# Kernel optimization log

Hardware: AMD Instinct MI355X
Metric: run time of the kernel (lower is better)

The kernel has to match this reference:

```python
import math
import jax, jax.numpy as jnp
import numpy as np

N_KV = 8
GROUP = 4
HEAD_DIM = 128
BATCH = 512
CACHE = 2048
CONTEXT = 4096
NEG_INF = -10000.0


def setup_inputs() -> dict:
    key = jax.random.key(0)
    k = jax.random.split(key, 6)
    queries = jax.random.normal(k[0], (N_KV * GROUP, BATCH, HEAD_DIM), jnp.float32)
    keys = jax.random.normal(k[1], (N_KV, BATCH, HEAD_DIM), jnp.float32)
    key_t_caches = jax.random.normal(k[2], (N_KV, HEAD_DIM, CACHE), jnp.float32)
    values = jax.random.normal(k[3], (N_KV, BATCH, HEAD_DIM), jnp.float32)
    value_caches = jax.random.normal(k[4], (N_KV, CACHE, HEAD_DIM), jnp.float32)
    # causal bias: token b (global position CACHE+b) may attend to positions <= CACHE+b;
    # padded tail [CACHE+BATCH, CONTEXT) is always masked with NEG_INF
    pos = jnp.arange(CONTEXT)[None, :]                       # [1, CONTEXT]
    limit = (CACHE + jnp.arange(BATCH))[:, None]             # [BATCH, 1]
    attn_bias = jnp.where(pos <= limit, 0.0, NEG_INF).astype(jnp.float32)
    kq_scale = jnp.asarray([1.0 / math.sqrt(HEAD_DIM)], jnp.float32)
    return {
        "queries": queries,
        "keys": keys,
        "key_t_caches": key_t_caches,
        "values": values,
        "value_caches": value_caches,
        "attn_bias": attn_bias,
        "kq_scale": kq_scale,
    }


def reference(queries, keys, key_t_caches, values, value_caches, attn_bias, kq_scale):
    n_kv, B, D = keys.shape
    n_heads = queries.shape[0]
    group = n_heads // n_kv
    cache = key_t_caches.shape[-1]
    context = attn_bias.shape[-1]
    pad = context - cache - B

    scaled_keys = keys * kq_scale                            # [kv, B, D]
    scaled_values = jnp.maximum(values, NEG_INF)             # [kv, B, D]

    # pad new keys/values to fill context, then prepend cache (matches torch pad+cat)
    padded_kt = jnp.pad(scaled_keys.transpose(0, 2, 1), ((0, 0), (0, 0), (0, pad)))
    all_keys_t = jnp.concatenate([key_t_caches, padded_kt], axis=-1)   # [kv, D, context]
    padded_v = jnp.pad(scaled_values, ((0, 0), (0, pad), (0, 0)))
    all_values = jnp.concatenate([value_caches, padded_v], axis=1)     # [kv, context, D]

    q = queries.reshape(n_kv, group, B, D)                   # group-major per kv head
    scores = jnp.einsum('kgbd,kdc->kgbc', q, all_keys_t) + attn_bias   # [kv, g, B, context]
    probs = jax.nn.softmax(scores, axis=-1)
    out = jnp.einsum('kgbc,kcd->kgbd', probs, all_values)    # [kv, g, B, D]
    head_outs = out.reshape(n_heads, B, D)
    return head_outs, scaled_keys, scaled_values
```

## Files before the change

### kernel.cpp

```cpp
#include <hip/hip_runtime.h>
#include <hip/hip_bf16.h>

#define NKV 8
#define NHEADS 32
#define HDIM 128
#define BATCH 512
#define CACHE 2048
#define CTX_TOT 2560
#define CT 64
#define SPLITS 6
#define KPITCH 128
#define VPITCH 64
#define PPITCH 72
#define NEG_BIG (-1e30f)

typedef __attribute__((ext_vector_type(8))) _Float16 half8;
typedef __attribute__((ext_vector_type(4))) float floatx4;

static __device__ __forceinline__ void dma16(const void* g, void* l) {
    __builtin_amdgcn_global_load_lds((const __attribute__((address_space(1))) void*)g,
                                     (__attribute__((address_space(3))) void*)l,
                                     16, 0, 0);
}

__global__ __launch_bounds__(256) void prep(const float* __restrict__ ktc,
                                            const float* __restrict__ vc,
                                            const float* __restrict__ keys,
                                            const float* __restrict__ values,
                                            const float* __restrict__ kq,
                                            float* __restrict__ outk,
                                            float* __restrict__ outv,
                                            _Float16* __restrict__ Kh,
                                            _Float16* __restrict__ Vth) {
    __shared__ float tile[128 * 33];
    const int bid = blockIdx.x;
    const int t = threadIdx.x;

    if (bid < 512) {
        int c0 = (bid & 63) * 32, kv = bid >> 6;
        const float* src = ktc + (size_t)kv * HDIM * CACHE + c0;
#pragma unroll
        for (int i = 0; i < 4; i++) {
            int idx = t + 256 * i;
            int d = idx >> 3, cc = idx & 7;
            float4 v = *(const float4*)(src + (size_t)d * CACHE + cc * 4);
            *(float4*)(&tile[d * 33 + cc * 4]) = v;
        }
        __syncthreads();
        _Float16* dst = Kh + ((size_t)kv * CTX_TOT + c0) * HDIM;
#pragma unroll
        for (int i = 0; i < 2; i++) {
            int c = (t >> 4) + 16 * i, dg = t & 15;
            half8 o;
#pragma unroll
            for (int k = 0; k < 8; k++) o[k] = (_Float16)tile[(dg * 8 + k) * 33 + c];
            *(half8*)(dst + (size_t)c * HDIM + dg * 8) = o;
        }
    } else if (bid < 1024) {
        int l = bid - 512;
        int c1 = (l & 15) * 128, d0 = ((l >> 4) & 3) * 32, kv = l >> 6;
        const float* src = vc + ((size_t)kv * CACHE + c1) * HDIM + d0;
#pragma unroll
        for (int i = 0; i < 4; i++) {
            int idx = t + 256 * i;
            int c = idx >> 3, dc = idx & 7;
            float4 v = *(const float4*)(src + (size_t)c * HDIM + dc * 4);
            *(float4*)(&tile[c * 33 + dc * 4]) = v;
        }
        __syncthreads();
        _Float16* dst = Vth + ((size_t)kv * HDIM + d0) * CTX_TOT + c1;
#pragma unroll
        for (int i = 0; i < 2; i++) {
            int d = (t >> 4) + 16 * i, cg = t & 15;
            half8 o;
#pragma unroll
            for (int k = 0; k < 8; k++) o[k] = (_Float16)tile[(cg * 8 + k) * 33 + d];
            *(half8*)(dst + (size_t)d * CTX_TOT + cg * 8) = o;
        }
    } else if (bid < 1536) {
        int base = ((bid - 1024) * 256 + t) * 4;
        float s = kq[0];
        float4 v = *(const float4*)(keys + base);
        v.x *= s; v.y *= s; v.z *= s; v.w *= s;
        *(float4*)(outk + base) = v;
        int kv = base >> 16;
        int rem = base & 0xFFFF;
        _Float16* dst = Kh + ((size_t)kv * CTX_TOT + CACHE) * HDIM + rem;
        dst[0] = (_Float16)v.x; dst[1] = (_Float16)v.y;
        dst[2] = (_Float16)v.z; dst[3] = (_Float16)v.w;
    } else {
        int l = bid - 1536;
        int b1 = (l & 3) * 128, d0 = ((l >> 2) & 3) * 32, kv = l >> 4;
        const float* src = values + ((size_t)kv * BATCH + b1) * HDIM + d0;
        float* dst32 = outv + ((size_t)kv * BATCH + b1) * HDIM + d0;
#pragma unroll
        for (int i = 0; i < 4; i++) {
            int idx = t + 256 * i;
            int b = idx >> 3, dc = idx & 7;
            float4 v = *(const float4*)(src + (size_t)b * HDIM + dc * 4);
            v.x = fmaxf(v.x, -10000.0f); v.y = fmaxf(v.y, -10000.0f);
            v.z = fmaxf(v.z, -10000.0f); v.w = fmaxf(v.w, -10000.0f);
            *(float4*)(dst32 + (size_t)b * HDIM + dc * 4) = v;
            *(float4*)(&tile[b * 33 + dc * 4]) = v;
        }
        __syncthreads();
        _Float16* dst = Vth + ((size_t)kv * HDIM + d0) * CTX_TOT + CACHE + b1;
#pragma unroll
        for (int i = 0; i < 2; i++) {
            int d = (t >> 4) + 16 * i, bg = t & 15;
            half8 o;
#pragma unroll
            for (int k = 0; k < 8; k++) o[k] = (_Float16)tile[(bg * 8 + k) * 33 + d];
            *(half8*)(dst + (size_t)d * CTX_TOT + bg * 8) = o;
        }
    }
}

__global__ __launch_bounds__(256, 3) void attn_split(const float* __restrict__ q_g,
                                                     const _Float16* __restrict__ Kh,
                                                     const _Float16* __restrict__ Vth,
                                                     _Float16* __restrict__ Opart,
                                                     float* __restrict__ MLpart) {
    __shared__ _Float16 Klds[CT * KPITCH];
    __shared__ _Float16 Vlds[HDIM * VPITCH];
    __shared__ _Float16 Plds[4][32 * PPITCH];

    const int h = blockIdx.x & 31;
    const int qb2 = blockIdx.x >> 5;
    const int s = blockIdx.y;
    const int kv = h >> 2;
    const int t = threadIdx.x;
    const int wave = t >> 6;
    const int lane = t & 63;
    const int l15 = lane & 15, quad = lane >> 4;

    const float LOG2E = 1.44269504088896340736f;
    const int qrow0 = qb2 * 128 + wave * 16;

    const _Float16* kg = Kh + (size_t)kv * CTX_TOT * HDIM;
    const _Float16* vg = Vth + (size_t)kv * HDIM * CTX_TOT;

    half8 qfrag[2][4];
#pragma unroll
    for (int hh = 0; hh < 2; hh++) {
        const float* qp = q_g + ((size_t)h * BATCH + qrow0 + hh * 64 + l15) * HDIM + quad * 8;
#pragma unroll
        for (int kb = 0; kb < 4; kb++) {
            const float* p = qp + kb * 32;
            float4 a = *(const float4*)p;
            float4 b = *(const float4*)(p + 4);
            qfrag[hh][kb][0] = (_Float16)(a.x * LOG2E); qfrag[hh][kb][1] = (_Float16)(a.y * LOG2E);
            qfrag[hh][kb][2] = (_Float16)(a.z * LOG2E); qfrag[hh][kb][3] = (_Float16)(a.w * LOG2E);
            qfrag[hh][kb][4] = (_Float16)(b.x * LOG2E); qfrag[hh][kb][5] = (_Float16)(b.y * LOG2E);
            qfrag[hh][kb][6] = (_Float16)(b.z * LOG2E); qfrag[hh][kb][7] = (_Float16)(b.w * LOG2E);
        }
    }

    floatx4 O[2][8];
#pragma unroll
    for (int hh = 0; hh < 2; hh++)
#pragma unroll
        for (int nb = 0; nb < 8; nb++) O[hh][nb] = (floatx4){0.f, 0.f, 0.f, 0.f};
    float m_r[2][4], l_r[2][4];
#pragma unroll
    for (int hh = 0; hh < 2; hh++)
#pragma unroll
        for (int r = 0; r < 4; r++) { m_r[hh][r] = NEG_BIG; l_r[hh][r] = 0.f; }

    const int nT = 34 + 2 * qb2;

    for (int tt = s; tt < nT; tt += SPLITS) {
        const int c0 = tt * CT;
        __syncthreads();
#pragma unroll
        for (int j = 0; j < 4; j++) {
            int row = wave * 16 + j * 4 + (lane >> 4);
            int gch = (lane & 15) ^ (row & 7);
            dma16(kg + (size_t)(c0 + row) * HDIM + gch * 8,
                  &Klds[(wave * 16 + j * 4) * KPITCH]);
        }
#pragma unroll
        for (int j = 0; j < 4; j++) {
            int row = wave * 32 + j * 8 + (lane >> 3);
            int gch = (lane & 7) ^ (row & 7);
            dma16(vg + (size_t)row * CTX_TOT + c0 + gch * 8,
                  &Vlds[(wave * 32 + j * 8) * VPITCH]);
        }
        __syncthreads();

        if (c0 <= CACHE + qrow0 + 64 + 15) {
#pragma unroll
            for (int hh = 0; hh < 2; hh++) {
                const int qr0h = qrow0 + hh * 64;
                if (c0 <= CACHE + qr0h + 15) {
                    floatx4 S[4];
#pragma unroll
                    for (int cs = 0; cs < 4; cs++) {
                        floatx4 a0 = (floatx4){0.f, 0.f, 0.f, 0.f};
                        int crow = cs * 16 + l15;
#pragma unroll
                        for (int kb = 0; kb < 4; kb++) {
                            half8 kf = *(const half8*)(&Klds[crow * KPITCH +
                                                             (((kb * 4 + quad) ^ (crow & 7)) << 3)]);
                            a0 = __builtin_amdgcn_mfma_f32_16x16x32_f16(qfrag[hh][kb], kf, a0, 0, 0, 0);
                        }
                        S[cs] = a0;
                    }
                    if (c0 + CT > CACHE + qr0h) {
#pragma unroll
                        for (int cs = 0; cs < 4; cs++)
#pragma unroll
                            for (int r = 0; r < 4; r++) {
                                int c = c0 + cs * 16 + l15;
                                if (c > CACHE + qr0h + quad * 4 + r) S[cs][r] = NEG_BIG;
                            }
                    }
                    float tmax[4];
#pragma unroll
                    for (int r = 0; r < 4; r++)
                        tmax[r] = fmaxf(fmaxf(S[0][r], S[1][r]), fmaxf(S[2][r], S[3][r]));
#pragma unroll
                    for (int off = 8; off >= 1; off >>= 1)
#pragma unroll
                        for (int r = 0; r < 4; r++)
                            tmax[r] = fmaxf(tmax[r], __shfl_xor(tmax[r], off, 64));
                    bool ch = false;
#pragma unroll
                    for (int r = 0; r < 4; r++) ch = ch || (tmax[r] > m_r[hh][r]);
                    if (__any(ch)) {
#pragma unroll
                        for (int r = 0; r < 4; r++) {
                            float mn = fmaxf(m_r[hh][r], tmax[r]);
                            float alpha = __builtin_amdgcn_exp2f(m_r[hh][r] - mn);
                            m_r[hh][r] = mn;
                            l_r[hh][r] *= alpha;
#pragma unroll
                            for (int nb = 0; nb < 8; nb++) O[hh][nb][r] *= alpha;
                        }
                    }
#pragma unroll
                    for (int cs = 0; cs < 4; cs++)
#pragma unroll
                        for (int r = 0; r < 4; r++) {
                            float p = __builtin_amdgcn_exp2f(S[cs][r] - m_r[hh][r]);
                            l_r[hh][r] += p;
                            Plds[wave][(hh * 16 + quad * 4 + r) * PPITCH + cs * 16 + l15] = (_Float16)p;
                        }
                } else {
#pragma unroll
                    for (int cs = 0; cs < 4; cs++)
#pragma unroll
                        for (int r = 0; r < 4; r++)
                            Plds[wave][(hh * 16 + quad * 4 + r) * PPITCH + cs * 16 + l15] = (_Float16)0.f;
                }
            }
#pragma unroll
            for (int kb2 = 0; kb2 < 2; kb2++) {
                half8 pf0 = *(const half8*)(&Plds[wave][l15 * PPITCH + kb2 * 32 + quad * 8]);
                half8 pf1 = *(const half8*)(&Plds[wave][(16 + l15) * PPITCH + kb2 * 32 + quad * 8]);
#pragma unroll
                for (int nb = 0; nb < 8; nb++) {
                    int vrow = nb * 16 + l15;
                    half8 vf = *(const half8*)(&Vlds[vrow * VPITCH +
                                                     (((kb2 * 4 + quad) ^ (vrow & 7)) << 3)]);
                    O[0][nb] = __builtin_amdgcn_mfma_f32_16x16x32_f16(pf0, vf, O[0][nb], 0, 0, 0);
                    O[1][nb] = __builtin_amdgcn_mfma_f32_16x16x32_f16(pf1, vf, O[1][nb], 0, 0, 0);
                }
            }
        }
    }

#pragma unroll
    for (int hh = 0; hh < 2; hh++)
#pragma unroll
        for (int off = 8; off >= 1; off >>= 1)
#pragma unroll
            for (int r = 0; r < 4; r++) l_r[hh][r] += __shfl_xor(l_r[hh][r], off, 64);

    const size_t rowbase = (size_t)s * NHEADS * BATCH + (size_t)h * BATCH;
#pragma unroll
    for (int hh = 0; hh < 2; hh++) {
#pragma unroll
        for (int nb = 0; nb < 8; nb++)
#pragma unroll
            for (int r = 0; r < 4; r++) {
                int brow = qrow0 + hh * 64 + quad * 4 + r;
                Opart[(rowbase + brow) * HDIM + nb * 16 + l15] = (_Float16)O[hh][nb][r];
            }
        if (l15 == 0) {
#pragma unroll
            for (int r = 0; r < 4; r++) {
                int brow = qrow0 + hh * 64 + quad * 4 + r;
                MLpart[(rowbase + brow) * 2 + 0] = m_r[hh][r];
                MLpart[(rowbase + brow) * 2 + 1] = l_r[hh][r];
            }
        }
    }
}

__global__ __launch_bounds__(256) void attn_merge(const _Float16* __restrict__ Opart,
                                                  const float* __restrict__ MLpart,
                                                  float* __restrict__ out) {
    const int t = threadIdx.x;
    const int row = blockIdx.x * 2 + (t >> 7);
    const int d = t & 127;
    const size_t stride = (size_t)NHEADS * BATCH;

    float m[SPLITS], l[SPLITS];
    float mm = NEG_BIG;
#pragma unroll
    for (int s = 0; s < SPLITS; s++) {
        m[s] = MLpart[((size_t)s * stride + row) * 2];
        l[s] = MLpart[((size_t)s * stride + row) * 2 + 1];
        mm = fmaxf(mm, m[s]);
    }
    float denom = 0.f, acc = 0.f;
#pragma unroll
    for (int s = 0; s < SPLITS; s++) {
        float w = __builtin_amdgcn_exp2f(m[s] - mm);
        denom += w * l[s];
        acc += w * (float)Opart[((size_t)s * stride + row) * HDIM + d];
    }
    out[(size_t)row * HDIM + d] = acc / denom;
}

extern "C" void kernel_launch(void* const* d_in, const int* in_sizes, int n_in,
                              void* d_out, int out_size, void* d_ws, size_t ws_size,
                              hipStream_t stream) {
    const float* queries = (const float*)d_in[0];
    const float* keys    = (const float*)d_in[1];
    const float* ktc     = (const float*)d_in[2];
    const float* values  = (const float*)d_in[3];
    const float* vcache  = (const float*)d_in[4];
    const float* kq      = (const float*)d_in[6];

    float* out     = (float*)d_out;
    float* out_sk  = out + (size_t)NHEADS * BATCH * HDIM;
    float* out_sv  = out_sk + (size_t)NKV * BATCH * HDIM;

    _Float16* Kh   = (_Float16*)d_ws;
    _Float16* Vth  = Kh + (size_t)NKV * CTX_TOT * HDIM;
    _Float16* Opart = Vth + (size_t)NKV * HDIM * CTX_TOT;
    float*    MLpart = (float*)(Opart + (size_t)SPLITS * NHEADS * BATCH * HDIM);

    prep<<<dim3(1664), dim3(256), 0, stream>>>(ktc, vcache, keys, values, kq,
                                               out_sk, out_sv, Kh, Vth);
    attn_split<<<dim3(128, SPLITS), dim3(256), 0, stream>>>(queries, Kh, Vth, Opart, MLpart);
    attn_merge<<<dim3(8192), dim3(256), 0, stream>>>(Opart, MLpart, out);
}
```

Baseline: 146.4 us.

## Double-buffer K/V tiles in LDS with halved context tile size

Halves the context tile from 64 to 32 columns and adds a second LDS buffer for K and V. The async global-to-LDS copy for the next tile now overlaps with the MFMA and softmax work on the current tile, and each iteration needs one barrier instead of two. LDS use stays roughly the same, so occupancy should hold. In exchange there are twice as many iterations with smaller MFMA batches, more frequent online-softmax rescaling and reductions, and a narrower swizzle on V.

After: 152.9 us. 4.5% more time.

```diff
diff --git a/kernel.cpp b/kernel.cpp
--- a/kernel.cpp
+++ b/kernel.cpp
@@ -7,11 +7,9 @@
 #define BATCH 512
 #define CACHE 2048
 #define CTX_TOT 2560
-#define CT 64
+#define CT 32
 #define SPLITS 6
-#define KPITCH 128
-#define VPITCH 64
-#define PPITCH 72
+#define PP 40
 #define NEG_BIG (-1e30f)
 
 typedef __attribute__((ext_vector_type(8))) _Float16 half8;
@@ -121,9 +119,9 @@
                                                      const _Float16* __restrict__ Vth,
                                                      _Float16* __restrict__ Opart,
                                                      float* __restrict__ MLpart) {
-    __shared__ _Float16 Klds[CT * KPITCH];
-    __shared__ _Float16 Vlds[HDIM * VPITCH];
-    __shared__ _Float16 Plds[4][32 * PPITCH];
+    __shared__ _Float16 Klds[2][CT * 128];
+    __shared__ _Float16 Vlds[2][128 * CT];
+    __shared__ _Float16 Plds[4][32 * PP];
 
     const int h = blockIdx.x & 31;
     const int qb2 = blockIdx.x >> 5;
@@ -167,48 +165,55 @@
 #pragma unroll
         for (int r = 0; r < 4; r++) { m_r[hh][r] = NEG_BIG; l_r[hh][r] = 0.f; }
 
-    const int nT = 34 + 2 * qb2;
+    const int nT = 68 + 4 * qb2;
+
+    auto stage = [&](int ttile, int b) {
+        const int c0s = ttile * CT;
+#pragma unroll
+        for (int j = 0; j < 2; j++) {
+            int row = wave * 8 + j * 4 + (lane >> 4);
+            int gch = (lane & 15) ^ (row & 7);
+            dma16(kg + (size_t)(c0s + row) * HDIM + gch * 8,
+                  &Klds[b][(wave * 8 + j * 4) * 128]);
+        }
+#pragma unroll
+        for (int j = 0; j < 2; j++) {
+            int row = wave * 32 + j * 16 + (lane >> 2);
+            int gch = (lane & 3) ^ (row & 3);
+            dma16(vg + (size_t)row * CTX_TOT + c0s + gch * 8,
+                  &Vlds[b][(wave * 32 + j * 16) * CT]);
+        }
+    };
+
+    stage(s, 0);
+    __syncthreads();
+    int buf = 0;
 
     for (int tt = s; tt < nT; tt += SPLITS) {
         const int c0 = tt * CT;
-        __syncthreads();
-#pragma unroll
-        for (int j = 0; j < 4; j++) {
-            int row = wave * 16 + j * 4 + (lane >> 4);
-            int gch = (lane & 15) ^ (row & 7);
-            dma16(kg + (size_t)(c0 + row) * HDIM + gch * 8,
-                  &Klds[(wave * 16 + j * 4) * KPITCH]);
-        }
-#pragma unroll
-        for (int j = 0; j < 4; j++) {
-            int row = wave * 32 + j * 8 + (lane >> 3);
-            int gch = (lane & 7) ^ (row & 7);
-            dma16(vg + (size_t)row * CTX_TOT + c0 + gch * 8,
-                  &Vlds[(wave * 32 + j * 8) * VPITCH]);
-        }
-        __syncthreads();
+        if (tt + SPLITS < nT) stage(tt + SPLITS, buf ^ 1);
 
         if (c0 <= CACHE + qrow0 + 64 + 15) {
 #pragma unroll
             for (int hh = 0; hh < 2; hh++) {
                 const int qr0h = qrow0 + hh * 64;
                 if (c0 <= CACHE + qr0h + 15) {
-                    floatx4 S[4];
-#pragma unroll
-                    for (int cs = 0; cs < 4; cs++) {
+                    floatx4 S[2];
+#pragma unroll
+                    for (int cs = 0; cs < 2; cs++) {
                         floatx4 a0 = (floatx4){0.f, 0.f, 0.f, 0.f};
                         int crow = cs * 16 + l15;
 #pragma unroll
                         for (int kb = 0; kb < 4; kb++) {
-                            half8 kf = *(const half8*)(&Klds[crow * KPITCH +
-                                                             (((kb * 4 + quad) ^ (crow & 7)) << 3)]);
+                            half8 kf = *(const half8*)(&Klds[buf][crow * 128 +
+                                                       (((kb * 4 + quad) ^ (crow & 7)) << 3)]);
                             a0 = __builtin_amdgcn_mfma_f32_16x16x32_f16(qfrag[hh][kb], kf, a0, 0, 0, 0);
                         }
                         S[cs] = a0;
                     }
                     if (c0 + CT > CACHE + qr0h) {
 #pragma unroll
-                        for (int cs = 0; cs < 4; cs++)
+                        for (int cs = 0; cs < 2; cs++)
 #pragma unroll
                             for (int r = 0; r < 4; r++) {
                                 int c = c0 + cs * 16 + l15;
@@ -218,7 +223,7 @@
                     float tmax[4];
 #pragma unroll
                     for (int r = 0; r < 4; r++)
-                        tmax[r] = fmaxf(fmaxf(S[0][r], S[1][r]), fmaxf(S[2][r], S[3][r]));
+                        tmax[r] = fmaxf(S[0][r], S[1][r]);
 #pragma unroll
                     for (int off = 8; off >= 1; off >>= 1)
 #pragma unroll
@@ -239,35 +244,37 @@
                         }
                     }
 #pragma unroll
-                    for (int cs = 0; cs < 4; cs++)
+                    for (int cs = 0; cs < 2; cs++)
 #pragma unroll
                         for (int r = 0; r < 4; r++) {
                             float p = __builtin_amdgcn_exp2f(S[cs][r] - m_r[hh][r]);
                             l_r[hh][r] += p;
-                            Plds[wave][(hh * 16 + quad * 4 + r) * PPITCH + cs * 16 + l15] = (_Float16)p;
+                            Plds[wave][(hh * 16 + quad * 4 + r) * PP + cs * 16 + l15] = (_Float16)p;
                         }
                 } else {
 #pragma unroll
-                    for (int cs = 0; cs < 4; cs++)
+                    for (int cs = 0; cs < 2; cs++)
 #pragma unroll
                         for (int r = 0; r < 4; r++)
-                            Plds[wave][(hh * 16 + quad * 4 + r) * PPITCH + cs * 16 + l15] = (_Float16)0.f;
+                            Plds[wave][(hh * 16 + quad * 4 + r) * PP + cs * 16 + l15] = (_Float16)0.f;
                 }
             }
-#pragma unroll
-            for (int kb2 = 0; kb2 < 2; kb2++) {
-                half8 pf0 = *(const half8*)(&Plds[wave][l15 * PPITCH + kb2 * 32 + quad * 8]);
-                half8 pf1 = *(const half8*)(&Plds[wave][(16 + l15) * PPITCH + kb2 * 32 + quad * 8]);
+            {
+                half8 pf0 = *(const half8*)(&Plds[wave][l15 * PP + quad * 8]);
+                half8 pf1 = *(const half8*)(&Plds[wave][(16 + l15) * PP + quad * 8]);
 #pragma unroll
                 for (int nb = 0; nb < 8; nb++) {
                     int vrow = nb * 16 + l15;
-                    half8 vf = *(const half8*)(&Vlds[vrow * VPITCH +
-                                                     (((kb2 * 4 + quad) ^ (vrow & 7)) << 3)]);
+                    half8 vf = *(const half8*)(&Vlds[buf][vrow * CT +
+                                                         ((quad ^ (vrow & 3)) << 3)]);
                     O[0][nb] = __builtin_amdgcn_mfma_f32_16x16x32_f16(pf0, vf, O[0][nb], 0, 0, 0);
                     O[1][nb] = __builtin_amdgcn_mfma_f32_16x16x32_f16(pf1, vf, O[1][nb], 0, 0, 0);
                 }
             }
         }
+
+        __syncthreads();
+        buf ^= 1;
     }
 
 #pragma unroll
```
